# Kernel tuning notes

Measured on AMD Instinct MI355X. Metric: run time of the kernel, lower is better.

## Reference

```python
import jax, jax.numpy as jnp
import numpy as np

B, S, HID = 2, 2048, 2048
H = 16
HD = HID // H            # 128
HD2 = HD // 2            # 64 (rope dim per head)
LAT = HID // 8           # 256 latent dim
BASE = 10000.0


def _rotary_table(seq_len):
    # inv_freq over rope dim HD2
    inv_freq = 1.0 / (BASE ** (jnp.arange(0, HD2, 2, dtype=jnp.float32) / HD2))  # [HD2//2]
    pos = jnp.arange(seq_len, dtype=jnp.float32)
    sincos = pos[:, None] * inv_freq[None, :]                 # [S, HD2//2]
    return jnp.concatenate([jnp.sin(sincos), jnp.cos(sincos)], axis=-1)  # [S, HD2]


def _apply_rope(x, emb):
    # x: [B, S, H, HD2]; emb: [S, HD2]
    half = HD2 // 2
    x1, x2 = x[..., :half], x[..., half:]
    sin = emb[None, :, None, :half]
    cos = emb[None, :, None, half:]
    return jnp.concatenate([x1 * cos - x2 * sin, x1 * sin + x2 * cos], axis=-1)


def setup_inputs() -> dict:
    key = jax.random.key(0)
    ks = jax.random.split(key, 9)
    s = 0.02
    return {
        "hidden_states": jax.random.normal(ks[0], (B, S, HID), jnp.float32),
        "w_kv_d": jax.random.normal(ks[1], (HID, LAT), jnp.float32) * s,
        "w_q_d": jax.random.normal(ks[2], (HID, LAT), jnp.float32) * s,
        "w_k_u": jax.random.normal(ks[3], (LAT, H * HD2), jnp.float32) * s,
        "w_q_u": jax.random.normal(ks[4], (LAT, H * HD2), jnp.float32) * s,
        "w_v_u": jax.random.normal(ks[5], (LAT, H * HD), jnp.float32) * s,
        "w_rope_k": jax.random.normal(ks[6], (HID, HID // 2), jnp.float32) * s,
        "w_rope_q": jax.random.normal(ks[7], (LAT, HID // 2), jnp.float32) * s,
        "w_o": jax.random.normal(ks[8], (HID, HID), jnp.float32) * s,
    }


def reference(hidden_states, w_kv_d, w_q_d, w_k_u, w_q_u, w_v_u, w_rope_k, w_rope_q, w_o):
    b, s, _ = hidden_states.shape
    kv_d = hidden_states @ w_kv_d            # [B,S,LAT]
    q_d = hidden_states @ w_q_d              # [B,S,LAT]
    k_p = (kv_d @ w_k_u).reshape(b, s, H, HD2)
    q_p = (q_d @ w_q_u).reshape(b, s, H, HD2)
    v = (kv_d @ w_v_u).reshape(b, s, H, HD)
    k_r = (hidden_states @ w_rope_k).reshape(b, s, H, HD2)
    q_r = (q_d @ w_rope_q).reshape(b, s, H, HD2)

    emb = _rotary_table(s)
    k_r = _apply_rope(k_r, emb)
    q_r = _apply_rope(q_r, emb)

    k = jnp.concatenate([k_p, k_r], axis=-1)  # [B,S,H,HD]
    q = jnp.concatenate([q_p, q_r], axis=-1)

    scores = jnp.einsum('bqhd,bkhd->bhqk', q, k) / jnp.sqrt(jnp.float32(HD))
    causal = jnp.tril(jnp.ones((s, s), dtype=bool))
    scores = jnp.where(causal[None, None], scores, jnp.float32(-1e9))
    probs = jax.nn.softmax(scores, axis=-1)
    out = jnp.einsum('bhqk,bkhd->bqhd', probs, v).reshape(b, s, HID)
    return out @ w_o
```

## Files before the change

kernel.cpp:

```cpp
#include <hip/hip_runtime.h>
#include <hip/hip_bf16.h>

#define BB 2
#define SS 2048
#define HID 2048
#define NH 16
#define BS (BB*SS)
#define SCALE 0.088388347648318447f

typedef __bf16 bf16x8 __attribute__((ext_vector_type(8)));
typedef float f32x4 __attribute__((ext_vector_type(4)));

__device__ __forceinline__ bf16x8 ld_frag(const __hip_bfloat16* p) {
    uint4 u = *reinterpret_cast<const uint4*>(p);
    return __builtin_bit_cast(bf16x8, u);
}
__device__ __forceinline__ void store_c(__hip_bfloat16* C, size_t idx, float v) {
    C[idx] = __float2bfloat16(v);
}
__device__ __forceinline__ void store_c(float* C, size_t idx, float v) {
    C[idx] = v;
}
__device__ __forceinline__ ushort bf_bits(float v) {
    __hip_bfloat16 h = __float2bfloat16(v);
    return *reinterpret_cast<ushort*>(&h);
}

#define GLD16(gp, lp) \
  __builtin_amdgcn_global_load_lds((const __attribute__((address_space(1))) void*)(gp), \
                                   (__attribute__((address_space(3))) void*)(lp), 16, 0, 0)

__global__ __launch_bounds__(256) void convert_kernel(
    const float* __restrict__ src, __hip_bfloat16* __restrict__ dst, int n8)
{
    int i = blockIdx.x * blockDim.x + threadIdx.x;
    if (i >= n8) return;
    float4 a = reinterpret_cast<const float4*>(src)[2 * i];
    float4 b = reinterpret_cast<const float4*>(src)[2 * i + 1];
    ushort u[8] = { bf_bits(a.x), bf_bits(a.y), bf_bits(a.z), bf_bits(a.w),
                    bf_bits(b.x), bf_bits(b.y), bf_bits(b.z), bf_bits(b.w) };
    reinterpret_cast<uint4*>(dst)[i] = *reinterpret_cast<uint4*>(u);
}

__global__ __launch_bounds__(256) void transpose_weights_kernel(
    const float* s0, const float* s1, const float* s2, const float* s3,
    const float* s4, const float* s5, const float* s6, const float* s7,
    __hip_bfloat16* WT1, __hip_bfloat16* WT2, __hip_bfloat16* WT3,
    __hip_bfloat16* WTo)
{
    const float* srcs[8] = { s0, s1, s2, s3, s4, s5, s6, s7 };
    const int Rs[8] = { 2048, 2048, 2048, 256, 256, 256, 256, 2048 };
    const int Cs[8] = { 256, 256, 1024, 1024, 2048, 1024, 1024, 2048 };
    __hip_bfloat16* dsts[8] = {
        WT1, WT1 + (size_t)256 * 2048, WT1 + (size_t)512 * 2048,
        WT2, WT2 + (size_t)1024 * 256,
        WT3, WT3 + (size_t)1024 * 256,
        WTo };
    const int prefix[9] = { 0, 512, 1024, 3072, 3328, 3840, 4096, 4352, 8448 };

    int bid = blockIdx.x;
    int seg = 0;
    #pragma unroll
    for (int i = 0; i < 8; i++) if (bid >= prefix[i + 1]) seg = i + 1;
    int local = bid - prefix[seg];
    int R = Rs[seg], C = Cs[seg];
    int tilesC = C / 32;
    int tr = local / tilesC, tc = local % tilesC;
    int r0 = tr * 32, c0 = tc * 32;
    const float* src = srcs[seg];
    __hip_bfloat16* dst = dsts[seg];

    __shared__ float Ts[32][33];
    int t = threadIdx.x;
    int ty = t >> 5, tx = t & 31;
    #pragma unroll
    for (int k = 0; k < 4; k++) {
        int r = ty + k * 8;
        Ts[r][tx] = src[(size_t)(r0 + r) * C + c0 + tx];
    }
    __syncthreads();
    #pragma unroll
    for (int k = 0; k < 4; k++) {
        int r = ty + k * 8;
        dst[(size_t)(c0 + r) * R + r0 + tx] = __float2bfloat16(Ts[tx][r]);
    }
}

template <typename TC>
__global__ __launch_bounds__(256) void gemm_bt_kernel(
    const __hip_bfloat16* __restrict__ A, int lda,
    const __hip_bfloat16* __restrict__ Bt,
    TC* __restrict__ C0, int ldc0, int sp0, int off0,
    TC* __restrict__ C1, int ldc1, int sp1, int off1,
    int splitN, int K)
{
    __shared__ alignas(16) __hip_bfloat16 As[128 * 32];
    __shared__ alignas(16) __hip_bfloat16 Bs[128 * 32];

    const int bn = blockIdx.x * 128;
    const int bm = blockIdx.y * 128;
    const int t = threadIdx.x;
    const int w = t >> 6;
    const int lane = t & 63;
    const int l15 = lane & 15;
    const int quad = lane >> 4;
    const int wm = (w & 1) * 64;
    const int wn = (w >> 1) * 64;

    const int srow = lane >> 2;
    const int skcol = (lane & 3) * 8;

    f32x4 acc[4][4] = {};

    for (int k0 = 0; k0 < K; k0 += 32) {
        __syncthreads();
        #pragma unroll
        for (int i = 0; i < 2; i++) {
            int r = w * 32 + i * 16 + srow;
            GLD16(A + (size_t)(bm + r) * lda + k0 + skcol, &As[r * 32 + skcol]);
            GLD16(Bt + (size_t)(bn + r) * K + k0 + skcol, &Bs[r * 32 + skcol]);
        }
        __syncthreads();

        bf16x8 af[4], bf[4];
        #pragma unroll
        for (int mt = 0; mt < 4; mt++)
            af[mt] = ld_frag(&As[(wm + mt * 16 + l15) * 32 + quad * 8]);
        #pragma unroll
        for (int nt = 0; nt < 4; nt++)
            bf[nt] = ld_frag(&Bs[(wn + nt * 16 + l15) * 32 + quad * 8]);
        #pragma unroll
        for (int mt = 0; mt < 4; mt++)
            #pragma unroll
            for (int nt = 0; nt < 4; nt++)
                acc[mt][nt] = __builtin_amdgcn_mfma_f32_16x16x32_bf16(
                    af[mt], bf[nt], acc[mt][nt], 0, 0, 0);
    }

    #pragma unroll
    for (int nt = 0; nt < 4; nt++) {
        int col = bn + wn + nt * 16 + l15;
        TC* Cp; int c, ld, s64, off;
        if (col < splitN) { Cp = C0; c = col; ld = ldc0; s64 = sp0; off = off0; }
        else { Cp = C1; c = col - splitN; ld = ldc1; s64 = sp1; off = off1; }
        if (s64 == 2) {
            #pragma unroll
            for (int mt = 0; mt < 4; mt++) {
                int row0 = bm + wm + mt * 16 + quad * 4;
                #pragma unroll
                for (int r = 0; r < 4; r++)
                    store_c(Cp, (size_t)c * 4096 + row0 + r, acc[mt][nt][r]);
            }
        } else {
            int oc = s64 ? ((c >> 6) * 128 + (c & 63) + off) : c;
            #pragma unroll
            for (int mt = 0; mt < 4; mt++) {
                #pragma unroll
                for (int r = 0; r < 4; r++) {
                    int row = bm + wm + mt * 16 + quad * 4 + r;
                    store_c(Cp, (size_t)row * ld + oc, acc[mt][nt][r]);
                }
            }
        }
    }
}

__global__ __launch_bounds__(256) void rope_kernel(
    __hip_bfloat16* __restrict__ Kb, __hip_bfloat16* __restrict__ Qb)
{
    int idx = blockIdx.x * blockDim.x + threadIdx.x;
    if (idx >= BS * NH * 32) return;
    int i = idx & 31;
    int h = (idx >> 5) & 15;
    int row = idx >> 9;
    int s = row & (SS - 1);

    float inv = exp2f(-(float)i * 0.4152410118609203f);
    float ang = (float)s * inv;
    float sn = sinf(ang), cs = cosf(ang);

    size_t obase = (size_t)row * 2048 + h * 128 + 64 + i;
    {
        float x1 = __bfloat162float(Kb[obase]);
        float x2 = __bfloat162float(Kb[obase + 32]);
        Kb[obase]      = __float2bfloat16(x1 * cs - x2 * sn);
        Kb[obase + 32] = __float2bfloat16(x1 * sn + x2 * cs);
    }
    {
        float x1 = __bfloat162float(Qb[obase]);
        float x2 = __bfloat162float(Qb[obase + 32]);
        Qb[obase]      = __float2bfloat16(x1 * cs - x2 * sn);
        Qb[obase + 32] = __float2bfloat16(x1 * sn + x2 * cs);
    }
}

__global__ __launch_bounds__(256) void flash_attn_kernel(
    const __hip_bfloat16* __restrict__ Q,
    const __hip_bfloat16* __restrict__ Kb,
    const __hip_bfloat16* __restrict__ Vt,
    __hip_bfloat16* __restrict__ O)
{
    __shared__ alignas(16) __hip_bfloat16 Kt[4 * 64 * 32];
    __shared__ alignas(16) __hip_bfloat16 Vs[2 * 128 * 32];
    __shared__ alignas(16) __hip_bfloat16 Sp[4][32 * 72];

    const int bxq = (gridDim.x - 1) - blockIdx.x;
    const int h = blockIdx.y;
    const int b = blockIdx.z;
    const int t = threadIdx.x;
    const int w = t >> 6;
    const int lane = t & 63;
    const int l15 = lane & 15;
    const int quad = lane >> 4;
    const int qbase = bxq * 128;

    const __hip_bfloat16* Kbase = Kb + (size_t)(b * SS) * 2048 + h * 128;
    const __hip_bfloat16* Vtb = Vt + (size_t)(h * 128) * 4096 + b * SS;

    bf16x8 qf[2][4];
    #pragma unroll
    for (int qs = 0; qs < 2; qs++) {
        const __hip_bfloat16* qrow =
            Q + (size_t)(b * SS + qbase + w * 32 + qs * 16 + l15) * 2048 + h * 128;
        #pragma unroll
        for (int ds = 0; ds < 4; ds++)
            qf[qs][ds] = ld_frag(qrow + ds * 32 + quad * 8);
    }

    float m_i[2] = { -INFINITY, -INFINITY };
    float l_i[2] = { 0.0f, 0.0f };
    f32x4 acc[2][8] = {};

    const int Lr = lane >> 2;
    const int Lc = (lane & 3) ^ (Lr & 3);
    const int kvh_w = w >> 1, dh_w = w & 1;
    const int ntiles = 2 * bxq + 2;

    for (int kt = 0; kt < ntiles; kt++) {
        const int kvbase = kt * 64;
        __syncthreads();

        #pragma unroll
        for (int i = 0; i < 4; i++) {
            GLD16(Kbase + (size_t)(kvbase + i * 16 + Lr) * 2048 + w * 32 + Lc * 8,
                  &Kt[w * 2048 + i * 512 + lane * 8]);
        }
        #pragma unroll
        for (int i = 0; i < 4; i++) {
            GLD16(Vtb + (size_t)(dh_w * 64 + i * 16 + Lr) * 4096
                      + kvbase + kvh_w * 32 + Lc * 8,
                  &Vs[kvh_w * 4096 + dh_w * 2048 + i * 512 + lane * 8]);
        }
        __syncthreads();

        f32x4 st[4][2];
        #pragma unroll
        for (int kvsub = 0; kvsub < 4; kvsub++) {
            st[kvsub][0] = f32x4{};
            st[kvsub][1] = f32x4{};
            #pragma unroll
            for (int ds = 0; ds < 4; ds++) {
                bf16x8 kf = ld_frag(&Kt[ds * 2048 + (kvsub * 16 + l15) * 32
                                        + (quad ^ (l15 & 3)) * 8]);
                #pragma unroll
                for (int qs = 0; qs < 2; qs++)
                    st[kvsub][qs] = __builtin_amdgcn_mfma_f32_16x16x32_bf16(
                        kf, qf[qs][ds], st[kvsub][qs], 0, 0, 0);
            }
        }
        #pragma unroll
        for (int qs = 0; qs < 2; qs++) {
            int q = qbase + w * 32 + qs * 16 + l15;
            #pragma unroll
            for (int kvsub = 0; kvsub < 4; kvsub++) {
                #pragma unroll
                for (int r = 0; r < 4; r++) {
                    int kv = kvbase + kvsub * 16 + quad * 4 + r;
                    st[kvsub][qs][r] = (kv <= q) ? st[kvsub][qs][r] * SCALE
                                                 : -INFINITY;
                }
            }
        }

        float alpha[2];
        #pragma unroll
        for (int qs = 0; qs < 2; qs++) {
            float tm = st[0][qs][0];
            #pragma unroll
            for (int kvsub = 0; kvsub < 4; kvsub++)
                #pragma unroll
                for (int r = 0; r < 4; r++) tm = fmaxf(tm, st[kvsub][qs][r]);
            tm = fmaxf(tm, __shfl_xor(tm, 16));
            tm = fmaxf(tm, __shfl_xor(tm, 32));
            float mnew = fmaxf(m_i[qs], tm);
            float rs = 0.0f;
            #pragma unroll
            for (int kvsub = 0; kvsub < 4; kvsub++)
                #pragma unroll
                for (int r = 0; r < 4; r++) {
                    float pv = __expf(st[kvsub][qs][r] - mnew);
                    st[kvsub][qs][r] = pv;
                    rs += pv;
                }
            rs += __shfl_xor(rs, 16);
            rs += __shfl_xor(rs, 32);
            alpha[qs] = __expf(m_i[qs] - mnew);
            m_i[qs] = mnew;
            l_i[qs] = l_i[qs] * alpha[qs] + rs;
        }

        #pragma unroll
        for (int qs = 0; qs < 2; qs++) {
            #pragma unroll
            for (int kvsub = 0; kvsub < 4; kvsub++) {
                ushort pk[4] = { bf_bits(st[kvsub][qs][0]), bf_bits(st[kvsub][qs][1]),
                                 bf_bits(st[kvsub][qs][2]), bf_bits(st[kvsub][qs][3]) };
                *reinterpret_cast<uint2*>(
                    &Sp[w][(qs * 16 + l15) * 72 + kvsub * 16 + quad * 4]) =
                    *reinterpret_cast<uint2*>(pk);
            }
        }

        #pragma unroll
        for (int qs = 0; qs < 2; qs++) {
            float al[4];
            #pragma unroll
            for (int r = 0; r < 4; r++) al[r] = __shfl(alpha[qs], quad * 4 + r, 64);
            #pragma unroll
            for (int dt = 0; dt < 8; dt++)
                #pragma unroll
                for (int r = 0; r < 4; r++) acc[qs][dt][r] *= al[r];
        }

        #pragma unroll
        for (int kvh = 0; kvh < 2; kvh++) {
            bf16x8 pf[2];
            #pragma unroll
            for (int qs = 0; qs < 2; qs++)
                pf[qs] = ld_frag(&Sp[w][(qs * 16 + l15) * 72 + kvh * 32 + quad * 8]);
            #pragma unroll
            for (int dt = 0; dt < 8; dt++) {
                bf16x8 vf = ld_frag(&Vs[kvh * 4096 + (dt * 16 + l15) * 32
                                        + (quad ^ (l15 & 3)) * 8]);
                #pragma unroll
                for (int qs = 0; qs < 2; qs++)
                    acc[qs][dt] = __builtin_amdgcn_mfma_f32_16x16x32_bf16(
                        pf[qs], vf, acc[qs][dt], 0, 0, 0);
            }
        }
    }

    #pragma unroll
    for (int qs = 0; qs < 2; qs++) {
        float li[4];
        #pragma unroll
        for (int r = 0; r < 4; r++) li[r] = __shfl(l_i[qs], quad * 4 + r, 64);
        #pragma unroll
        for (int r = 0; r < 4; r++) {
            int row = qbase + w * 32 + qs * 16 + quad * 4 + r;
            __hip_bfloat16* orow = O + (size_t)(b * SS + row) * 2048 + h * 128;
            float inv_l = 1.0f / li[r];
            #pragma unroll
            for (int dt = 0; dt < 8; dt++)
                orow[dt * 16 + l15] = __float2bfloat16(acc[qs][dt][r] * inv_l);
        }
    }
}

extern "C" void kernel_launch(void* const* d_in, const int* in_sizes, int n_in,
                              void* d_out, int out_size, void* d_ws, size_t ws_size,
                              hipStream_t stream)
{
    const float* hs       = (const float*)d_in[0];
    const float* w_kv_d   = (const float*)d_in[1];
    const float* w_q_d    = (const float*)d_in[2];
    const float* w_k_u    = (const float*)d_in[3];
    const float* w_q_u    = (const float*)d_in[4];
    const float* w_v_u    = (const float*)d_in[5];
    const float* w_rope_k = (const float*)d_in[6];
    const float* w_rope_q = (const float*)d_in[7];
    const float* w_o      = (const float*)d_in[8];
    float* out = (float*)d_out;

    char* p = (char*)d_ws;
    auto alloc = [&](size_t nelem) {
        __hip_bfloat16* r = (__hip_bfloat16*)p;
        p += nelem * sizeof(__hip_bfloat16);
        return r;
    };
    __hip_bfloat16* hsb  = alloc((size_t)BS * HID);
    __hip_bfloat16* qkvd = alloc((size_t)BS * 512);
    __hip_bfloat16* WT1  = alloc((size_t)1536 * 2048);
    __hip_bfloat16* WT2  = alloc((size_t)3072 * 256);
    __hip_bfloat16* WT3  = alloc((size_t)2048 * 256);
    __hip_bfloat16* WTo  = alloc((size_t)2048 * 2048);
    __hip_bfloat16* Kbuf = alloc((size_t)BS * HID);
    __hip_bfloat16* Qbuf = alloc((size_t)BS * HID);
    __hip_bfloat16* Vtb  = alloc((size_t)HID * BS);
    __hip_bfloat16* attn = hsb;

    dim3 blk(256);

    convert_kernel<<<dim3((BS * HID / 8 + 255) / 256), blk, 0, stream>>>(
        hs, hsb, BS * HID / 8);
    transpose_weights_kernel<<<dim3(8448), blk, 0, stream>>>(
        w_kv_d, w_q_d, w_rope_k, w_k_u, w_v_u, w_q_u, w_rope_q, w_o,
        WT1, WT2, WT3, WTo);

    gemm_bt_kernel<__hip_bfloat16><<<dim3(1536 / 128, BS / 128), blk, 0, stream>>>(
        hsb, 2048, WT1,
        qkvd, 512, 0, 0,
        Kbuf, 2048, 1, 64,
        512, 2048);
    gemm_bt_kernel<__hip_bfloat16><<<dim3(3072 / 128, BS / 128), blk, 0, stream>>>(
        qkvd, 512, WT2,
        Kbuf, 2048, 1, 0,
        Vtb, 0, 2, 0,
        1024, 256);
    gemm_bt_kernel<__hip_bfloat16><<<dim3(2048 / 128, BS / 128), blk, 0, stream>>>(
        qkvd + 256, 512, WT3,
        Qbuf, 2048, 1, 0,
        Qbuf, 2048, 1, 64,
        1024, 256);
    rope_kernel<<<dim3((BS * NH * 32 + 255) / 256), blk, 0, stream>>>(Kbuf, Qbuf);
    flash_attn_kernel<<<dim3(SS / 128, NH, BB), blk, 0, stream>>>(
        Qbuf, Kbuf, Vtb, attn);
    gemm_bt_kernel<float><<<dim3(2048 / 128, BS / 128), blk, 0, stream>>>(
        attn, 2048, WTo,
        out, 2048, 0, 0,
        out, 2048, 0, 0,
        2048, 2048);
}
```

Before: 387.6 us.

## Skip fully masked KV tiles per wave, use exp2 softmax, and interleave batch order

Each wave now skips compute on KV tiles that lie entirely above its 32 query rows, and applies the causal mask only on diagonal tiles. Softmax folds log2(e) into the scale and uses exp2f, and probabilities are packed with paired bf16 conversions. Batch 1 processes query blocks in forward order while batch 0 keeps reverse order, to balance work across the grid. Waves that skip still take part in the shared loads and barriers, so the saving is limited to MFMA and exp work on the skipped tiles.

```diff
diff --git a/kernel.cpp b/kernel.cpp
--- a/kernel.cpp
+++ b/kernel.cpp
@@ -7,6 +7,7 @@
 #define NH 16
 #define BS (BB*SS)
 #define SCALE 0.088388347648318447f
+#define SCALE_L2E 0.12751744502911988f
 
 typedef __bf16 bf16x8 __attribute__((ext_vector_type(8)));
 typedef float f32x4 __attribute__((ext_vector_type(4)));
@@ -24,6 +25,10 @@
 __device__ __forceinline__ ushort bf_bits(float v) {
     __hip_bfloat16 h = __float2bfloat16(v);
     return *reinterpret_cast<ushort*>(&h);
+}
+__device__ __forceinline__ uint pack_bf2(float a, float b) {
+    __hip_bfloat162 h2 = __float22bfloat162_rn(float2{a, b});
+    return *reinterpret_cast<uint*>(&h2);
 }
 
 #define GLD16(gp, lp) \
@@ -204,7 +209,8 @@
     __shared__ alignas(16) __hip_bfloat16 Vs[2 * 128 * 32];
     __shared__ alignas(16) __hip_bfloat16 Sp[4][32 * 72];
 
-    const int bxq = (gridDim.x - 1) - blockIdx.x;
+    const int qx = blockIdx.x;
+    const int bxq = blockIdx.z ? qx : (gridDim.x - 1 - qx);
     const int h = blockIdx.y;
     const int b = blockIdx.z;
     const int t = threadIdx.x;
@@ -213,6 +219,8 @@
     const int l15 = lane & 15;
     const int quad = lane >> 4;
     const int qbase = bxq * 128;
+    const int qmin_w = qbase + w * 32;
+    const int qmax_w = qmin_w + 31;
 
     const __hip_bfloat16* Kbase = Kb + (size_t)(b * SS) * 2048 + h * 128;
     const __hip_bfloat16* Vtb = Vt + (size_t)(h * 128) * 4096 + b * SS;
@@ -221,7 +229,7 @@
     #pragma unroll
     for (int qs = 0; qs < 2; qs++) {
         const __hip_bfloat16* qrow =
-            Q + (size_t)(b * SS + qbase + w * 32 + qs * 16 + l15) * 2048 + h * 128;
+            Q + (size_t)(b * SS + qmin_w + qs * 16 + l15) * 2048 + h * 128;
         #pragma unroll
         for (int ds = 0; ds < 4; ds++)
             qf[qs][ds] = ld_frag(qrow + ds * 32 + quad * 8);
@@ -253,6 +261,8 @@
         }
         __syncthreads();
 
+        if (kvbase > qmax_w) continue;
+
         f32x4 st[4][2];
         #pragma unroll
         for (int kvsub = 0; kvsub < 4; kvsub++) {
@@ -268,18 +278,28 @@
                         kf, qf[qs][ds], st[kvsub][qs], 0, 0, 0);
             }
         }
-        #pragma unroll
-        for (int qs = 0; qs < 2; qs++) {
-            int q = qbase + w * 32 + qs * 16 + l15;
-            #pragma unroll
-            for (int kvsub = 0; kvsub < 4; kvsub++) {
-                #pragma unroll
-                for (int r = 0; r < 4; r++) {
-                    int kv = kvbase + kvsub * 16 + quad * 4 + r;
-                    st[kvsub][qs][r] = (kv <= q) ? st[kvsub][qs][r] * SCALE
-                                                 : -INFINITY;
+        if (kvbase + 63 > qmin_w) {
+            #pragma unroll
+            for (int qs = 0; qs < 2; qs++) {
+                int q = qmin_w + qs * 16 + l15;
+                #pragma unroll
+                for (int kvsub = 0; kvsub < 4; kvsub++) {
+                    #pragma unroll
+                    for (int r = 0; r < 4; r++) {
+                        int kv = kvbase + kvsub * 16 + quad * 4 + r;
+                        st[kvsub][qs][r] = (kv <= q) ? st[kvsub][qs][r] * SCALE_L2E
+                                                     : -INFINITY;
+                    }
                 }
             }
+        } else {
+            #pragma unroll
+            for (int kvsub = 0; kvsub < 4; kvsub++)
+                #pragma unroll
+                for (int qs = 0; qs < 2; qs++)
+                    #pragma unroll
+                    for (int r = 0; r < 4; r++)
+                        st[kvsub][qs][r] *= SCALE_L2E;
         }
 
         float alpha[2];
@@ -298,13 +318,13 @@
             for (int kvsub = 0; kvsub < 4; kvsub++)
                 #pragma unroll
                 for (int r = 0; r < 4; r++) {
-                    float pv = __expf(st[kvsub][qs][r] - mnew);
+                    float pv = exp2f(st[kvsub][qs][r] - mnew);
                     st[kvsub][qs][r] = pv;
                     rs += pv;
                 }
             rs += __shfl_xor(rs, 16);
             rs += __shfl_xor(rs, 32);
-            alpha[qs] = __expf(m_i[qs] - mnew);
+            alpha[qs] = exp2f(m_i[qs] - mnew);
             m_i[qs] = mnew;
             l_i[qs] = l_i[qs] * alpha[qs] + rs;
         }
@@ -313,11 +333,10 @@
         for (int qs = 0; qs < 2; qs++) {
             #pragma unroll
             for (int kvsub = 0; kvsub < 4; kvsub++) {
-                ushort pk[4] = { bf_bits(st[kvsub][qs][0]), bf_bits(st[kvsub][qs][1]),
-                                 bf_bits(st[kvsub][qs][2]), bf_bits(st[kvsub][qs][3]) };
+                uint2 pk = { pack_bf2(st[kvsub][qs][0], st[kvsub][qs][1]),
+                             pack_bf2(st[kvsub][qs][2], st[kvsub][qs][3]) };
                 *reinterpret_cast<uint2*>(
-                    &Sp[w][(qs * 16 + l15) * 72 + kvsub * 16 + quad * 4]) =
-                    *reinterpret_cast<uint2*>(pk);
+                    &Sp[w][(qs * 16 + l15) * 72 + kvsub * 16 + quad * 4]) = pk;
             }
         }
 
@@ -357,7 +376,7 @@
         for (int r = 0; r < 4; r++) li[r] = __shfl(l_i[qs], quad * 4 + r, 64);
         #pragma unroll
         for (int r = 0; r < 4; r++) {
-            int row = qbase + w * 32 + qs * 16 + quad * 4 + r;
+            int row = qmin_w + qs * 16 + quad * 4 + r;
             __hip_bfloat16* orow = O + (size_t)(b * SS + row) * 2048 + h * 128;
             float inv_l = 1.0f / li[r];
             #pragma unroll
```

Measured after the change: 429.7 us. +10.9%, slower.
